# Performance work log

Hardware: AMD Instinct MI355X
Metric: run time of the kernel (lower is better)

Reference implementation:

```python
import jax, jax.numpy as jnp
import numpy as np
from jax import lax

EPS = 1e-5  # torch LayerNorm / BatchNorm1d default eps
HEADS, DH, DEPTH, C = 4, 128, 2, 512


def setup_inputs() -> dict:
    key = jax.random.key(0)
    ks = iter(jax.random.split(key, 48))
    def rn(shape, scale=1.0):
        return jax.random.normal(next(ks), shape, jnp.float32) * scale
    d, L = 1024, DEPTH
    inp = {}
    inp['x'] = rn((16, 10, 256, d))                      # (b, ncrops, T, d)
    # Temporal embedding: Conv1d(d -> 512, k=3, pad=1) + ReLU
    inp['W_emb'] = rn((C, d, 3), (d * 3) ** -0.5)
    inp['b_emb'] = jnp.zeros((C,), jnp.float32)
    # Transformer (depth=2), params stacked along layer axis
    inp['ln1_g'] = jnp.ones((L, C), jnp.float32); inp['ln1_b'] = jnp.zeros((L, C), jnp.float32)
    inp['W_qkv'] = rn((L, C, 4 * HEADS * DH), C ** -0.5)  # to_qkv (no bias), inner_dim*4 = 2048
    inp['W_o']  = rn((L, 2 * HEADS * DH, C), (2 * HEADS * DH) ** -0.5)
    inp['b_o']  = jnp.zeros((L, C), jnp.float32)
    inp['ln2_g'] = jnp.ones((L, C), jnp.float32); inp['ln2_b'] = jnp.zeros((L, C), jnp.float32)
    inp['W_f1'] = rn((L, C, C), C ** -0.5); inp['b_f1'] = jnp.zeros((L, C), jnp.float32)
    inp['W_f2'] = rn((L, C, C), C ** -0.5); inp['b_f2'] = jnp.zeros((L, C), jnp.float32)
    # NormalHead: conv1 512->32 (k=1), bn1, conv2 32->16 (k=1), bn2, conv3 16->1 (k=1)
    inp['c1_W'] = rn((32, C), C ** -0.5); inp['c1_b'] = jnp.zeros((32,), jnp.float32)
    inp['bn1_g'] = jnp.ones((32,), jnp.float32); inp['bn1_b'] = jnp.zeros((32,), jnp.float32)
    inp['bn1_m'] = rn((32,), 0.1)
    inp['bn1_v'] = jax.random.uniform(next(ks), (32,), jnp.float32, 0.5, 1.5)
    inp['c2_W'] = rn((16, 32), 32 ** -0.5); inp['c2_b'] = jnp.zeros((16,), jnp.float32)
    inp['bn2_g'] = jnp.ones((16,), jnp.float32); inp['bn2_b'] = jnp.zeros((16,), jnp.float32)
    inp['bn2_m'] = rn((16,), 0.1)
    inp['bn2_v'] = jax.random.uniform(next(ks), (16,), jnp.float32, 0.5, 1.5)
    inp['c3_W'] = rn((1, 16), 0.25); inp['c3_b'] = jnp.zeros((1,), jnp.float32)
    return inp


def _ln(z, g, b):
    m = z.mean(-1, keepdims=True)
    v = ((z - m) ** 2).mean(-1, keepdims=True)
    return (z - m) / jnp.sqrt(v + EPS) * g + b


def _bn_eval(z, g, b, m, v):  # z: (B, C, T), eval-mode BatchNorm1d
    return (z - m[None, :, None]) / jnp.sqrt(v[None, :, None] + EPS) * g[None, :, None] + b[None, :, None]


def _k1conv(z, W, b):  # pointwise Conv1d: z (B, Ci, T), W (Co, Ci)
    return jnp.einsum('bct,oc->bot', z, W) + b[None, :, None]


def reference(x, W_emb, b_emb, ln1_g, ln1_b, W_qkv, W_o, b_o, ln2_g, ln2_b,
              W_f1, b_f1, W_f2, b_f2, c1_W, c1_b, bn1_g, bn1_b, bn1_m, bn1_v,
              c2_W, c2_b, bn2_g, bn2_b, bn2_m, bn2_v, c3_W, c3_b):
    b, n, T, d = x.shape
    h = x.reshape(b * n, T, d)
    # Temporal embedding: Conv1d(k=3, pad=1) + ReLU
    h = lax.conv_general_dilated(h.transpose(0, 2, 1), W_emb, (1,), 'SAME',
                                 dimension_numbers=('NCH', 'OIH', 'NCH'))
    h = jax.nn.relu(h + b_emb[None, :, None]).transpose(0, 2, 1)  # (BN, T, 512)

    # fixed positional-decay attention map attn2 (T, T), batch-independent
    idx = jnp.arange(T, dtype=jnp.float32)
    tg = jnp.abs(idx[None, :] - idx[:, None])
    a2 = jnp.exp(-tg / jnp.exp(1.0))
    a2 = a2 / a2.sum(-1)  # NOTE: broadcast over last axis, exactly as in the torch code

    scale = DH ** -0.5
    for l in range(DEPTH):
        z = _ln(h, ln1_g[l], ln1_b[l])
        qkvt = z @ W_qkv[l]                                   # (BN, T, 2048)
        q, k, v, t = jnp.split(qkvt, 4, axis=-1)
        def to_heads(u):
            return u.reshape(u.shape[0], T, HEADS, DH).transpose(0, 2, 1, 3)
        q, k, v, t = map(to_heads, (q, k, v, t))              # (BN, H, T, DH)
        attn1 = jax.nn.softmax(jnp.einsum('bhid,bhjd->bhij', q, k) * scale, axis=-1)
        o1 = jnp.einsum('bhij,bhjd->bhid', attn1, v)
        o2 = jnp.einsum('ij,bhjd->bhid', a2, t)
        o = jnp.concatenate([o1, o2], axis=-1)                # (BN, H, T, 2*DH)
        o = o.transpose(0, 2, 1, 3).reshape(h.shape[0], T, HEADS * 2 * DH)
        h = o @ W_o[l] + b_o[l] + h                           # attn residual
        z = _ln(h, ln2_g[l], ln2_b[l])
        h = (jax.nn.gelu(z @ W_f1[l] + b_f1[l], approximate=False) @ W_f2[l] + b_f2[l]) + h

    # NormalHead on (BN, C, T)
    f = h.transpose(0, 2, 1)
    x1 = _k1conv(f, c1_W, c1_b)                               # (BN, 32, T)
    x2 = _k1conv(jax.nn.relu(_bn_eval(x1, bn1_g, bn1_b, bn1_m, bn1_v)), c2_W, c2_b)  # (BN, 16, T)
    scores = jax.nn.sigmoid(_k1conv(jax.nn.relu(_bn_eval(x2, bn2_g, bn2_b, bn2_m, bn2_v)), c3_W, c3_b))
    normal_scores = scores.reshape(b, n, T).mean(1)           # mean over ncrops -> (b, T)

    def maha(feats, anchor, var):  # Mahalanobis distance vs BN running stats (no eps, as in source)
        dist = jnp.sqrt(jnp.sum((feats - anchor[None, :, None]) ** 2 / var[None, :, None], axis=1))
        return dist.reshape(b, n, T).mean(1)

    distance_sum = maha(x1, bn1_m, bn1_v) + maha(x2, bn2_m, bn2_v)
    return distance_sum * normal_scores                       # (b, T)
```

## Files before the change

### kernel.cpp

```cpp
#include <hip/hip_runtime.h>
#include <math.h>

#define T_    256
#define D_    1024
#define C_    512
#define H_    4
#define DH_   128
#define BNB   160
#define LEPS  1e-5f
#define INV_E 0.36787944117144233f
#define SCALE_ 0.08838834764831845f
#define LDT   40

typedef unsigned short ushort;
typedef unsigned int   uint;
typedef __attribute__((ext_vector_type(8))) short short8;
typedef __attribute__((ext_vector_type(4))) float f32x4;

__device__ __forceinline__ ushort f2b(float f) {
    uint u = __float_as_uint(f);
    u += 0x7fffu + ((u >> 16) & 1u);
    return (ushort)(u >> 16);
}
__device__ __forceinline__ float b2f(ushort u) {
    return __uint_as_float(((uint)u) << 16);
}
__device__ __forceinline__ uint pk(float a, float b) {
    return (uint)f2b(a) | ((uint)f2b(b) << 16);
}

__global__ void zero_k(float* __restrict__ p, int n) {
    int i = blockIdx.x * 256 + threadIdx.x;
    if (i < n) p[i] = 0.0f;
}

__global__ void tconv_k(const float* __restrict__ src, ushort* __restrict__ dst,
                        int K, int N) {
    int idx = blockIdx.x * 256 + threadIdx.x;
    if (idx >= N * K) return;
    int n = idx / K, k = idx % K;
    dst[idx] = f2b(src[(size_t)k * N + n]);
}

__global__ void bcvt_k(const float* __restrict__ src, ushort* __restrict__ dst, int n) {
    int i = blockIdx.x * 256 + threadIdx.x;
    if (i < n) dst[i] = f2b(src[i]);
}

__global__ void wemb_k(const float* __restrict__ W, ushort* __restrict__ Wt) {
    int idx = blockIdx.x * 256 + threadIdx.x;
    if (idx >= C_ * 3072) return;
    int c = idx / 3072, k = idx % 3072;
    int dt = k >> 10, ci = k & 1023;
    Wt[idx] = f2b(W[(size_t)c * 3072 + ci * 3 + dt]);
}

__global__ void a2_colsum_k(float* __restrict__ s) {
    int j = threadIdx.x;
    float acc = 0.0f;
    for (int k = 0; k < T_; k++) acc += expf(-fabsf((float)(j - k)) * INV_E);
    s[j] = acc;
}

__global__ void a2fill_k(const float* __restrict__ s, ushort* __restrict__ A2) {
    int i = blockIdx.x, j = threadIdx.x;
    A2[i * 256 + j] = f2b(expf(-fabsf((float)(i - j)) * INV_E) / s[j]);
}

__global__ __launch_bounds__(256)
void ln_k(const float* __restrict__ X, const float* __restrict__ g,
          const float* __restrict__ b, ushort* __restrict__ Z) {
    int row = blockIdx.x;
    int tid = threadIdx.x;
    const float* xr = X + (size_t)row * C_;
    float x0 = xr[tid], x1 = xr[tid + 256];
    __shared__ float red[256];
    red[tid] = x0 + x1;
    __syncthreads();
    for (int s = 128; s >= 1; s >>= 1) {
        if (tid < s) red[tid] += red[tid + s];
        __syncthreads();
    }
    float mean = red[0] * (1.0f / C_);
    __syncthreads();
    float d0 = x0 - mean, d1 = x1 - mean;
    red[tid] = d0 * d0 + d1 * d1;
    __syncthreads();
    for (int s = 128; s >= 1; s >>= 1) {
        if (tid < s) red[tid] += red[tid + s];
        __syncthreads();
    }
    float rinv = rsqrtf(red[0] * (1.0f / C_) + LEPS);
    ushort* zr = Z + (size_t)row * C_;
    zr[tid]       = f2b(d0 * rinv * g[tid]       + b[tid]);
    zr[tid + 256] = f2b(d1 * rinv * g[tid + 256] + b[tid + 256]);
}

template<int CONV, int ACT, int RESID, int OUTBF>
__global__ __launch_bounds__(256)
void gemm_k(const ushort* __restrict__ A, const ushort* __restrict__ B,
            const float* __restrict__ bias, const float* __restrict__ R,
            void* __restrict__ Cout, int M, int N, int K,
            const float* __restrict__ Xf) {
    __shared__ __align__(16) ushort As[128 * LDT];
    __shared__ __align__(16) ushort Bs[128 * LDT];
    const int tid  = threadIdx.x;
    const int lane = tid & 63, wave = tid >> 6;
    const int wr = wave >> 1, wc = wave & 1;
    const int lm = lane & 15, quad = lane >> 4;
    const int m0 = blockIdx.y * 128, n0 = blockIdx.x * 128;
    const int r  = tid >> 1;
    const int c0 = (tid & 1) * 2;

    f32x4 acc[4][4];
#pragma unroll
    for (int mt = 0; mt < 4; mt++)
#pragma unroll
        for (int nt = 0; nt < 4; nt++) acc[mt][nt] = (f32x4){0.f, 0.f, 0.f, 0.f};

    for (int k0 = 0; k0 < K; k0 += 32) {
        if (CONV) {
            int g = m0 + r, bn = g >> 8, t = g & 255;
#pragma unroll
            for (int cc = 0; cc < 2; cc++) {
                int c = c0 + cc;
                int kc = k0 + c * 8;
                int dt = kc >> 10, ci = kc & 1023;
                int tt = t + dt - 1;
                uint4 val;
                if (tt >= 0 && tt < T_) {
                    const float* s = Xf + (size_t)(bn * T_ + tt) * D_ + ci;
                    float4 f0 = *(const float4*)s;
                    float4 f1 = *(const float4*)(s + 4);
                    val.x = pk(f0.x, f0.y); val.y = pk(f0.z, f0.w);
                    val.z = pk(f1.x, f1.y); val.w = pk(f1.z, f1.w);
                } else {
                    val.x = 0u; val.y = 0u; val.z = 0u; val.w = 0u;
                }
                *(uint4*)&As[r * LDT + c * 8] = val;
            }
        } else {
            const ushort* Arow = A + (size_t)(m0 + r) * K + k0;
            *(uint4*)&As[r * LDT + c0 * 8]       = *(const uint4*)(Arow + c0 * 8);
            *(uint4*)&As[r * LDT + (c0 + 1) * 8] = *(const uint4*)(Arow + (c0 + 1) * 8);
        }
        {
            const ushort* Brow = B + (size_t)(n0 + r) * K + k0;
            *(uint4*)&Bs[r * LDT + c0 * 8]       = *(const uint4*)(Brow + c0 * 8);
            *(uint4*)&Bs[r * LDT + (c0 + 1) * 8] = *(const uint4*)(Brow + (c0 + 1) * 8);
        }
        __syncthreads();
        short8 af[4], bfv[4];
#pragma unroll
        for (int mt = 0; mt < 4; mt++)
            af[mt] = *(const short8*)&As[(wr * 64 + mt * 16 + lm) * LDT + quad * 8];
#pragma unroll
        for (int nt = 0; nt < 4; nt++)
            bfv[nt] = *(const short8*)&Bs[(wc * 64 + nt * 16 + lm) * LDT + quad * 8];
#pragma unroll
        for (int mt = 0; mt < 4; mt++)
#pragma unroll
            for (int nt = 0; nt < 4; nt++)
                acc[mt][nt] = __builtin_amdgcn_mfma_f32_16x16x32_bf16(
                    af[mt], bfv[nt], acc[mt][nt], 0, 0, 0);
        __syncthreads();
    }

#pragma unroll
    for (int mt = 0; mt < 4; mt++) {
        int grow0 = m0 + wr * 64 + mt * 16 + quad * 4;
#pragma unroll
        for (int nt = 0; nt < 4; nt++) {
            int gcol = n0 + wc * 64 + nt * 16 + lm;
            float bia = bias ? bias[gcol] : 0.0f;
            f32x4 v = acc[mt][nt];
#pragma unroll
            for (int i = 0; i < 4; i++) {
                int grow = grow0 + i;
                float val = v[i] + bia;
                if (ACT == 1) val = val * 0.5f * (1.0f + erff(val * 0.70710678118654752f));
                if (ACT == 2) val = fmaxf(val, 0.0f);
                if (RESID) val += R[(size_t)grow * N + gcol];
                if (OUTBF) ((ushort*)Cout)[(size_t)grow * N + gcol] = f2b(val);
                else       ((float*)Cout)[(size_t)grow * N + gcol]  = val;
            }
        }
    }
}

__global__ __launch_bounds__(256)
void attn1_k(const ushort* __restrict__ qkvt, ushort* __restrict__ O) {
    const int bn = blockIdx.x, h = blockIdx.y;
    const int tid = threadIdx.x;
    const int wave = tid >> 6, lane = tid & 63;
    const int lm = lane & 15, quad = lane >> 4;
    __shared__ __align__(16) ushort Ks[32 * 136];
    __shared__ __align__(16) ushort Vt[128 * 40];
    __shared__ __align__(16) ushort Ps[4][64 * 40];
    const ushort* base = qkvt + (size_t)bn * T_ * 2048;

    short8 aq[4][4];
#pragma unroll
    for (int mt = 0; mt < 4; mt++) {
        const ushort* qrow = base + (size_t)(wave * 64 + mt * 16 + lm) * 2048 + h * DH_;
#pragma unroll
        for (int ks = 0; ks < 4; ks++)
            aq[mt][ks] = *(const short8*)(qrow + ks * 32 + quad * 8);
    }

    f32x4 oacc[4][8];
#pragma unroll
    for (int mt = 0; mt < 4; mt++)
#pragma unroll
        for (int nt = 0; nt < 8; nt++) oacc[mt][nt] = (f32x4){0.f, 0.f, 0.f, 0.f};
    float mrow[4][4], lrow[4][4];
#pragma unroll
    for (int mt = 0; mt < 4; mt++)
#pragma unroll
        for (int i = 0; i < 4; i++) { mrow[mt][i] = -1e30f; lrow[mt][i] = 0.0f; }

    for (int kt = 0; kt < 8; kt++) {
        __syncthreads();
#pragma unroll
        for (int u = 0; u < 2; u++) {
            int ii = tid + u * 256;
            int j = ii >> 4, dc = ii & 15;
            *(uint4*)&Ks[j * 136 + dc * 8] =
                *(const uint4*)(base + (size_t)(kt * 32 + j) * 2048 + 512 + h * DH_ + dc * 8);
        }
        {
            int j = tid & 31, half = tid >> 5;
            const ushort* vrow = base + (size_t)(kt * 32 + j) * 2048 + 1024 + h * DH_ + half * 16;
            uint4 v0 = *(const uint4*)vrow;
            uint4 v1 = *(const uint4*)(vrow + 8);
            ushort e[16];
            *(uint4*)&e[0] = v0; *(uint4*)&e[8] = v1;
#pragma unroll
            for (int u = 0; u < 16; u++)
                Vt[(half * 16 + u) * 40 + j] = e[u];
        }
        __syncthreads();

        f32x4 s[4][2];
#pragma unroll
        for (int mt = 0; mt < 4; mt++)
#pragma unroll
            for (int nt = 0; nt < 2; nt++) s[mt][nt] = (f32x4){0.f, 0.f, 0.f, 0.f};
#pragma unroll
        for (int ks = 0; ks < 4; ks++) {
            short8 bk0 = *(const short8*)&Ks[lm * 136 + ks * 32 + quad * 8];
            short8 bk1 = *(const short8*)&Ks[(16 + lm) * 136 + ks * 32 + quad * 8];
#pragma unroll
            for (int mt = 0; mt < 4; mt++) {
                s[mt][0] = __builtin_amdgcn_mfma_f32_16x16x32_bf16(aq[mt][ks], bk0, s[mt][0], 0, 0, 0);
                s[mt][1] = __builtin_amdgcn_mfma_f32_16x16x32_bf16(aq[mt][ks], bk1, s[mt][1], 0, 0, 0);
            }
        }

#pragma unroll
        for (int mt = 0; mt < 4; mt++) {
#pragma unroll
            for (int i = 0; i < 4; i++) {
                float v0 = s[mt][0][i] * SCALE_;
                float v1 = s[mt][1][i] * SCALE_;
                float rmax = fmaxf(v0, v1);
#pragma unroll
                for (int mk = 1; mk < 16; mk <<= 1)
                    rmax = fmaxf(rmax, __shfl_xor(rmax, mk));
                float mold = mrow[mt][i];
                float mnew = fmaxf(mold, rmax);
                float alpha = __expf(mold - mnew);
                float p0 = __expf(v0 - mnew);
                float p1 = __expf(v1 - mnew);
                float rs = p0 + p1;
#pragma unroll
                for (int mk = 1; mk < 16; mk <<= 1)
                    rs += __shfl_xor(rs, mk);
                lrow[mt][i] = lrow[mt][i] * alpha + rs;
                mrow[mt][i] = mnew;
#pragma unroll
                for (int nt = 0; nt < 8; nt++) {
                    oacc[mt][nt][i] *= alpha;
                }
                int prow = mt * 16 + quad * 4 + i;
                Ps[wave][prow * 40 + lm]      = f2b(p0);
                Ps[wave][prow * 40 + 16 + lm] = f2b(p1);
            }
        }

        short8 ap[4];
#pragma unroll
        for (int mt = 0; mt < 4; mt++)
            ap[mt] = *(const short8*)&Ps[wave][(mt * 16 + lm) * 40 + quad * 8];
#pragma unroll
        for (int nt = 0; nt < 8; nt++) {
            short8 bv = *(const short8*)&Vt[(nt * 16 + lm) * 40 + quad * 8];
#pragma unroll
            for (int mt = 0; mt < 4; mt++)
                oacc[mt][nt] = __builtin_amdgcn_mfma_f32_16x16x32_bf16(ap[mt], bv, oacc[mt][nt], 0, 0, 0);
        }
    }

#pragma unroll
    for (int mt = 0; mt < 4; mt++) {
#pragma unroll
        for (int i = 0; i < 4; i++) {
            int row = wave * 64 + mt * 16 + quad * 4 + i;
            float rinv = 1.0f / lrow[mt][i];
#pragma unroll
            for (int nt = 0; nt < 8; nt++) {
                int d = nt * 16 + lm;
                O[((size_t)bn * T_ + row) * 1024 + h * 256 + d] =
                    f2b(oacc[mt][nt][i] * rinv);
            }
        }
    }
}

__global__ __launch_bounds__(256)
void attn2_k(const ushort* __restrict__ A2, const ushort* __restrict__ qkvt,
             ushort* __restrict__ O) {
    __shared__ __align__(16) ushort As[128 * LDT];
    __shared__ __align__(16) ushort Bs[128 * 48];
    const int tid = threadIdx.x;
    const int bn = blockIdx.z;
    const int m0 = blockIdx.y * 128;
    const int n0 = blockIdx.x * 128;
    const int lane = tid & 63, wave = tid >> 6;
    const int wr = wave >> 1, wc = wave & 1;
    const int lm = lane & 15, quad = lane >> 4;
    const ushort* tbase = qkvt + (size_t)bn * T_ * 2048 + 1536;
    const int r = tid >> 1, c0 = (tid & 1) * 2;

    f32x4 acc[4][4];
#pragma unroll
    for (int mt = 0; mt < 4; mt++)
#pragma unroll
        for (int nt = 0; nt < 4; nt++) acc[mt][nt] = (f32x4){0.f, 0.f, 0.f, 0.f};

    for (int k0 = 0; k0 < 256; k0 += 32) {
        const ushort* Arow = A2 + (size_t)(m0 + r) * 256 + k0;
        *(uint4*)&As[r * LDT + c0 * 8]       = *(const uint4*)(Arow + c0 * 8);
        *(uint4*)&As[r * LDT + (c0 + 1) * 8] = *(const uint4*)(Arow + (c0 + 1) * 8);
        {
            int kr = tid & 31, np = tid >> 5;
            const ushort* trow = tbase + (size_t)(k0 + kr) * 2048 + n0 + np * 16;
            uint4 v0 = *(const uint4*)trow;
            uint4 v1 = *(const uint4*)(trow + 8);
            ushort e[16];
            *(uint4*)&e[0] = v0; *(uint4*)&e[8] = v1;
#pragma unroll
            for (int u = 0; u < 16; u++)
                Bs[(np * 16 + u) * 48 + kr] = e[u];
        }
        __syncthreads();
        short8 af[4], bf[4];
#pragma unroll
        for (int mt = 0; mt < 4; mt++)
            af[mt] = *(const short8*)&As[(wr * 64 + mt * 16 + lm) * LDT + quad * 8];
#pragma unroll
        for (int nt = 0; nt < 4; nt++)
            bf[nt] = *(const short8*)&Bs[(wc * 64 + nt * 16 + lm) * 48 + quad * 8];
#pragma unroll
        for (int mt = 0; mt < 4; mt++)
#pragma unroll
            for (int nt = 0; nt < 4; nt++)
                acc[mt][nt] = __builtin_amdgcn_mfma_f32_16x16x32_bf16(
                    af[mt], bf[nt], acc[mt][nt], 0, 0, 0);
        __syncthreads();
    }

#pragma unroll
    for (int mt = 0; mt < 4; mt++) {
        int row0 = m0 + wr * 64 + mt * 16 + quad * 4;
#pragma unroll
        for (int nt = 0; nt < 4; nt++) {
            int n = n0 + wc * 64 + nt * 16 + lm;
            int h = n >> 7, d = n & 127;
#pragma unroll
            for (int i = 0; i < 4; i++) {
                int row = row0 + i;
                O[((size_t)bn * T_ + row) * 1024 + h * 256 + 128 + d] =
                    f2b(acc[mt][nt][i]);
            }
        }
    }
}

#define BLD 520
__global__ __launch_bounds__(256)
void head1_k(const float* __restrict__ Hf, const ushort* __restrict__ c1Wb,
             const float* __restrict__ c1b, float* __restrict__ X1) {
    __shared__ __align__(16) ushort As[128 * LDT];
    __shared__ __align__(16) ushort Bs[32 * BLD];
    const int tid = threadIdx.x;
    const int lane = tid & 63, wave = tid >> 6;
    const int lm = lane & 15, quad = lane >> 4;
    const int m0 = blockIdx.x * 128;
#pragma unroll
    for (int u = 0; u < 8; u++) {
        int ii = tid + u * 256;
        int nrow = ii >> 6;
        int koff = (ii & 63) * 8;
        *(uint4*)&Bs[nrow * BLD + koff] = *(const uint4*)(c1Wb + nrow * 512 + koff);
    }
    f32x4 acc[2][2];
#pragma unroll
    for (int mt = 0; mt < 2; mt++)
#pragma unroll
        for (int nt = 0; nt < 2; nt++) acc[mt][nt] = (f32x4){0.f, 0.f, 0.f, 0.f};

    const int r = tid >> 1, half = tid & 1;
    for (int k0 = 0; k0 < 512; k0 += 32) {
        const float* s = Hf + (size_t)(m0 + r) * 512 + k0 + half * 16;
        float4 f0 = *(const float4*)s;
        float4 f1 = *(const float4*)(s + 4);
        float4 f2 = *(const float4*)(s + 8);
        float4 f3 = *(const float4*)(s + 12);
        uint4 v0, v1;
        v0.x = pk(f0.x, f0.y); v0.y = pk(f0.z, f0.w);
        v0.z = pk(f1.x, f1.y); v0.w = pk(f1.z, f1.w);
        v1.x = pk(f2.x, f2.y); v1.y = pk(f2.z, f2.w);
        v1.z = pk(f3.x, f3.y); v1.w = pk(f3.z, f3.w);
        __syncthreads();
        *(uint4*)&As[r * LDT + half * 16]     = v0;
        *(uint4*)&As[r * LDT + half * 16 + 8] = v1;
        __syncthreads();
        short8 af[2], bf[2];
#pragma unroll
        for (int mt = 0; mt < 2; mt++)
            af[mt] = *(const short8*)&As[(wave * 32 + mt * 16 + lm) * LDT + quad * 8];
#pragma unroll
        for (int nt = 0; nt < 2; nt++)
            bf[nt] = *(const short8*)&Bs[(nt * 16 + lm) * BLD + k0 + quad * 8];
#pragma unroll
        for (int mt = 0; mt < 2; mt++)
#pragma unroll
            for (int nt = 0; nt < 2; nt++)
                acc[mt][nt] = __builtin_amdgcn_mfma_f32_16x16x32_bf16(
                    af[mt], bf[nt], acc[mt][nt], 0, 0, 0);
    }
#pragma unroll
    for (int mt = 0; mt < 2; mt++) {
        int row0 = m0 + wave * 32 + mt * 16 + quad * 4;
#pragma unroll
        for (int nt = 0; nt < 2; nt++) {
            int col = nt * 16 + lm;
            float bia = c1b[col];
#pragma unroll
            for (int i = 0; i < 4; i++)
                X1[(size_t)(row0 + i) * 32 + col] = acc[mt][nt][i] + bia;
        }
    }
}

__global__ __launch_bounds__(256)
void head2_k(const float* __restrict__ X1, int bn_base, int M,
             const float* __restrict__ g1, const float* __restrict__ b1,
             const float* __restrict__ m1, const float* __restrict__ v1,
             const float* __restrict__ c2W, const float* __restrict__ c2b,
             const float* __restrict__ g2, const float* __restrict__ b2,
             const float* __restrict__ m2, const float* __restrict__ v2,
             const float* __restrict__ c3W, const float* __restrict__ c3b,
             float* __restrict__ sum_dist, float* __restrict__ sum_score) {
    int row = blockIdx.x * 256 + threadIdx.x;
    if (row >= M) return;
    float x1[32], y1[32];
    const float* xr = X1 + (size_t)row * 32;
#pragma unroll
    for (int c = 0; c < 32; c++) x1[c] = xr[c];
    float d1 = 0.0f;
#pragma unroll
    for (int c = 0; c < 32; c++) {
        float dd = x1[c] - m1[c];
        d1 += dd * dd / v1[c];
        y1[c] = fmaxf(0.0f, dd * rsqrtf(v1[c] + LEPS) * g1[c] + b1[c]);
    }
    float d2 = 0.0f, sc = c3b[0];
#pragma unroll
    for (int o = 0; o < 16; o++) {
        float acc = c2b[o];
        const float* wr = c2W + o * 32;
#pragma unroll
        for (int c = 0; c < 32; c++) acc += wr[c] * y1[c];
        float dd = acc - m2[o];
        d2 += dd * dd / v2[o];
        float y2 = fmaxf(0.0f, dd * rsqrtf(v2[o] + LEPS) * g2[o] + b2[o]);
        sc += c3W[o] * y2;
    }
    float dist = sqrtf(d1) + sqrtf(d2);
    sc = 1.0f / (1.0f + expf(-sc));
    int bn = bn_base + (row >> 8);
    int t = row & 255;
    int b = bn / 10;
    atomicAdd(&sum_dist[b * T_ + t], dist);
    atomicAdd(&sum_score[b * T_ + t], sc);
}

__global__ void combine_k(const float* __restrict__ sd, const float* __restrict__ ss,
                          float* __restrict__ out) {
    int i = blockIdx.x * 256 + threadIdx.x;
    if (i < 16 * T_) out[i] = (sd[i] * 0.1f) * (ss[i] * 0.1f);
}

extern "C" void kernel_launch(void* const* d_in, const int* in_sizes, int n_in,
                              void* d_out, int out_size, void* d_ws, size_t ws_size,
                              hipStream_t stream) {
    const float* x     = (const float*)d_in[0];
    const float* W_emb = (const float*)d_in[1];
    const float* b_emb = (const float*)d_in[2];
    const float* ln1_g = (const float*)d_in[3];
    const float* ln1_b = (const float*)d_in[4];
    const float* W_qkv = (const float*)d_in[5];
    const float* W_o   = (const float*)d_in[6];
    const float* b_o   = (const float*)d_in[7];
    const float* ln2_g = (const float*)d_in[8];
    const float* ln2_b = (const float*)d_in[9];
    const float* W_f1  = (const float*)d_in[10];
    const float* b_f1  = (const float*)d_in[11];
    const float* W_f2  = (const float*)d_in[12];
    const float* b_f2  = (const float*)d_in[13];
    const float* c1_W  = (const float*)d_in[14];
    const float* c1_b  = (const float*)d_in[15];
    const float* bn1_g = (const float*)d_in[16];
    const float* bn1_b = (const float*)d_in[17];
    const float* bn1_m = (const float*)d_in[18];
    const float* bn1_v = (const float*)d_in[19];
    const float* c2_W  = (const float*)d_in[20];
    const float* c2_b  = (const float*)d_in[21];
    const float* bn2_g = (const float*)d_in[22];
    const float* bn2_b = (const float*)d_in[23];
    const float* bn2_m = (const float*)d_in[24];
    const float* bn2_v = (const float*)d_in[25];
    const float* c3_W  = (const float*)d_in[26];
    const float* c3_b  = (const float*)d_in[27];
    float* out = (float*)d_out;

    char* p = (char*)d_ws;
    auto alloc = [&](size_t bytes) -> char* {
        char* q = p; p += (bytes + 255) & ~(size_t)255; return q;
    };
    ushort* wEmb = (ushort*)alloc((size_t)C_ * 3072 * 2);
    ushort* wQkv = (ushort*)alloc((size_t)2 * 2048 * 512 * 2);
    ushort* wO   = (ushort*)alloc((size_t)2 * 512 * 1024 * 2);
    ushort* wF1  = (ushort*)alloc((size_t)2 * 512 * 512 * 2);
    ushort* wF2  = (ushort*)alloc((size_t)2 * 512 * 512 * 2);
    ushort* A2bf = (ushort*)alloc((size_t)256 * 256 * 2);
    ushort* c1Wb = (ushort*)alloc((size_t)32 * 512 * 2);
    float*  s256      = (float*)alloc(256 * 4);
    float*  sum_dist  = (float*)alloc(4096 * 4);
    float*  sum_score = (float*)alloc(4096 * 4);
    size_t fixedB = (size_t)(p - (char*)d_ws);

    int CH = 8;
    const int cands[7] = {160, 80, 40, 32, 20, 16, 10};
    for (int ci = 0; ci < 7; ci++) {
        size_t per = (size_t)cands[ci] * 256 * 9344 + 4096;
        if (fixedB + per <= ws_size) { CH = cands[ci]; break; }
    }
    const int MR = CH * 256;
    float*  h    = (float*)alloc((size_t)MR * 512 * 4);
    ushort* z    = (ushort*)alloc((size_t)MR * 512 * 2);
    ushort* qkvt = (ushort*)alloc((size_t)MR * 2048 * 2);
    ushort* o    = (ushort*)alloc((size_t)MR * 1024 * 2);
    ushort* g    = o;
    float*  X1   = (float*)alloc((size_t)MR * 32 * 4);

    zero_k<<<(8192 + 255) / 256, 256, 0, stream>>>(sum_dist, 8192);
    a2_colsum_k<<<1, 256, 0, stream>>>(s256);
    a2fill_k<<<256, 256, 0, stream>>>(s256, A2bf);
    wemb_k<<<(C_ * 3072 + 255) / 256, 256, 0, stream>>>(W_emb, wEmb);
    bcvt_k<<<(32 * 512 + 255) / 256, 256, 0, stream>>>(c1_W, c1Wb, 32 * 512);
    for (int l = 0; l < 2; l++) {
        tconv_k<<<(2048 * 512 + 255) / 256, 256, 0, stream>>>(
            W_qkv + (size_t)l * 512 * 2048, wQkv + (size_t)l * 2048 * 512, 512, 2048);
        tconv_k<<<(512 * 1024 + 255) / 256, 256, 0, stream>>>(
            W_o + (size_t)l * 1024 * 512, wO + (size_t)l * 512 * 1024, 1024, 512);
        tconv_k<<<(512 * 512 + 255) / 256, 256, 0, stream>>>(
            W_f1 + (size_t)l * 512 * 512, wF1 + (size_t)l * 512 * 512, 512, 512);
        tconv_k<<<(512 * 512 + 255) / 256, 256, 0, stream>>>(
            W_f2 + (size_t)l * 512 * 512, wF2 + (size_t)l * 512 * 512, 512, 512);
    }

    for (int cs = 0; cs < BNB; cs += CH) {
        const float* xc = x + (size_t)cs * T_ * D_;

        gemm_k<1, 2, 0, 0><<<dim3(512 / 128, MR / 128), 256, 0, stream>>>(
            nullptr, wEmb, b_emb, nullptr, h, MR, 512, 3072, xc);

        for (int l = 0; l < 2; l++) {
            ln_k<<<MR, 256, 0, stream>>>(h, ln1_g + l * C_, ln1_b + l * C_, z);
            gemm_k<0, 0, 0, 1><<<dim3(2048 / 128, MR / 128), 256, 0, stream>>>(
                z, wQkv + (size_t)l * 2048 * 512, nullptr, nullptr, qkvt,
                MR, 2048, 512, nullptr);
            attn1_k<<<dim3(CH, H_), 256, 0, stream>>>(qkvt, o);
            attn2_k<<<dim3(4, 2, CH), 256, 0, stream>>>(A2bf, qkvt, o);
            gemm_k<0, 0, 1, 0><<<dim3(512 / 128, MR / 128), 256, 0, stream>>>(
                o, wO + (size_t)l * 512 * 1024, b_o + l * C_, h, h,
                MR, 512, 1024, nullptr);
            ln_k<<<MR, 256, 0, stream>>>(h, ln2_g + l * C_, ln2_b + l * C_, z);
            gemm_k<0, 1, 0, 1><<<dim3(512 / 128, MR / 128), 256, 0, stream>>>(
                z, wF1 + (size_t)l * 512 * 512, b_f1 + l * C_, nullptr, g,
                MR, 512, 512, nullptr);
            gemm_k<0, 0, 1, 0><<<dim3(512 / 128, MR / 128), 256, 0, stream>>>(
                g, wF2 + (size_t)l * 512 * 512, b_f2 + l * C_, h, h,
                MR, 512, 512, nullptr);
        }

        head1_k<<<MR / 128, 256, 0, stream>>>(h, c1Wb, c1_b, X1);
        head2_k<<<MR / 256, 256, 0, stream>>>(
            X1, cs, MR, bn1_g, bn1_b, bn1_m, bn1_v,
            c2_W, c2_b, bn2_g, bn2_b, bn2_m, bn2_v, c3_W, c3_b,
            sum_dist, sum_score);
    }

    combine_k<<<16, 256, 0, stream>>>(sum_dist, sum_score, out);
}
```

Measured before the change: 1.947 ms.

## Store residual stream in bf16 and pre-convert input x to bf16

The hidden-state residual buffer h becomes bf16 instead of fp32, so LayerNorm, the residual GEMM epilogues and head1 read and write half the bytes. The input x is converted to bf16 once per chunk by a new vectorized kernel, so the conv-embedding GEMM no longer re-reads and re-converts fp32 x for each of its three taps and every N tile. The trade-off is an extra full pass over x and a larger workspace, plus lower precision in the residual accumulation, which could affect accuracy.

```diff
diff --git a/kernel.cpp b/kernel.cpp
--- a/kernel.cpp
+++ b/kernel.cpp
@@ -34,6 +34,17 @@
     if (i < n) p[i] = 0.0f;
 }
 
+__global__ void xcvt_k(const float* __restrict__ src, ushort* __restrict__ dst, int n4) {
+    int i = blockIdx.x * 256 + threadIdx.x;
+    if (i < n4) {
+        float4 f = ((const float4*)src)[i];
+        uint2 v;
+        v.x = pk(f.x, f.y);
+        v.y = pk(f.z, f.w);
+        ((uint2*)dst)[i] = v;
+    }
+}
+
 __global__ void tconv_k(const float* __restrict__ src, ushort* __restrict__ dst,
                         int K, int N) {
     int idx = blockIdx.x * 256 + threadIdx.x;
@@ -68,12 +79,12 @@
 }
 
 __global__ __launch_bounds__(256)
-void ln_k(const float* __restrict__ X, const float* __restrict__ g,
+void ln_k(const ushort* __restrict__ X, const float* __restrict__ g,
           const float* __restrict__ b, ushort* __restrict__ Z) {
     int row = blockIdx.x;
     int tid = threadIdx.x;
-    const float* xr = X + (size_t)row * C_;
-    float x0 = xr[tid], x1 = xr[tid + 256];
+    const ushort* xr = X + (size_t)row * C_;
+    float x0 = b2f(xr[tid]), x1 = b2f(xr[tid + 256]);
     __shared__ float red[256];
     red[tid] = x0 + x1;
     __syncthreads();
@@ -99,9 +110,9 @@
 template<int CONV, int ACT, int RESID, int OUTBF>
 __global__ __launch_bounds__(256)
 void gemm_k(const ushort* __restrict__ A, const ushort* __restrict__ B,
-            const float* __restrict__ bias, const float* __restrict__ R,
+            const float* __restrict__ bias, const ushort* __restrict__ R,
             void* __restrict__ Cout, int M, int N, int K,
-            const float* __restrict__ Xf) {
+            const ushort* __restrict__ Xb) {
     __shared__ __align__(16) ushort As[128 * LDT];
     __shared__ __align__(16) ushort Bs[128 * LDT];
     const int tid  = threadIdx.x;
@@ -129,11 +140,7 @@
                 int tt = t + dt - 1;
                 uint4 val;
                 if (tt >= 0 && tt < T_) {
-                    const float* s = Xf + (size_t)(bn * T_ + tt) * D_ + ci;
-                    float4 f0 = *(const float4*)s;
-                    float4 f1 = *(const float4*)(s + 4);
-                    val.x = pk(f0.x, f0.y); val.y = pk(f0.z, f0.w);
-                    val.z = pk(f1.x, f1.y); val.w = pk(f1.z, f1.w);
+                    val = *(const uint4*)(Xb + ((size_t)bn * T_ + tt) * D_ + ci);
                 } else {
                     val.x = 0u; val.y = 0u; val.z = 0u; val.w = 0u;
                 }
@@ -180,7 +187,7 @@
                 float val = v[i] + bia;
                 if (ACT == 1) val = val * 0.5f * (1.0f + erff(val * 0.70710678118654752f));
                 if (ACT == 2) val = fmaxf(val, 0.0f);
-                if (RESID) val += R[(size_t)grow * N + gcol];
+                if (RESID) val += b2f(R[(size_t)grow * N + gcol]);
                 if (OUTBF) ((ushort*)Cout)[(size_t)grow * N + gcol] = f2b(val);
                 else       ((float*)Cout)[(size_t)grow * N + gcol]  = val;
             }
@@ -389,7 +396,7 @@
 
 #define BLD 520
 __global__ __launch_bounds__(256)
-void head1_k(const float* __restrict__ Hf, const ushort* __restrict__ c1Wb,
+void head1_k(const ushort* __restrict__ Hb, const ushort* __restrict__ c1Wb,
              const float* __restrict__ c1b, float* __restrict__ X1) {
     __shared__ __align__(16) ushort As[128 * LDT];
     __shared__ __align__(16) ushort Bs[32 * BLD];
@@ -412,16 +419,9 @@
 
     const int r = tid >> 1, half = tid & 1;
     for (int k0 = 0; k0 < 512; k0 += 32) {
-        const float* s = Hf + (size_t)(m0 + r) * 512 + k0 + half * 16;
-        float4 f0 = *(const float4*)s;
-        float4 f1 = *(const float4*)(s + 4);
-        float4 f2 = *(const float4*)(s + 8);
-        float4 f3 = *(const float4*)(s + 12);
-        uint4 v0, v1;
-        v0.x = pk(f0.x, f0.y); v0.y = pk(f0.z, f0.w);
-        v0.z = pk(f1.x, f1.y); v0.w = pk(f1.z, f1.w);
-        v1.x = pk(f2.x, f2.y); v1.y = pk(f2.z, f2.w);
-        v1.z = pk(f3.x, f3.y); v1.w = pk(f3.z, f3.w);
+        const ushort* s = Hb + (size_t)(m0 + r) * 512 + k0 + half * 16;
+        uint4 v0 = *(const uint4*)s;
+        uint4 v1 = *(const uint4*)(s + 8);
         __syncthreads();
         *(uint4*)&As[r * LDT + half * 16]     = v0;
         *(uint4*)&As[r * LDT + half * 16 + 8] = v1;
@@ -555,11 +555,12 @@
     int CH = 8;
     const int cands[7] = {160, 80, 40, 32, 20, 16, 10};
     for (int ci = 0; ci < 7; ci++) {
-        size_t per = (size_t)cands[ci] * 256 * 9344 + 4096;
+        size_t per = (size_t)cands[ci] * 256 * 10368 + 8192;
         if (fixedB + per <= ws_size) { CH = cands[ci]; break; }
     }
     const int MR = CH * 256;
-    float*  h    = (float*)alloc((size_t)MR * 512 * 4);
+    ushort* xb   = (ushort*)alloc((size_t)MR * 1024 * 2);
+    ushort* h    = (ushort*)alloc((size_t)MR * 512 * 2);
     ushort* z    = (ushort*)alloc((size_t)MR * 512 * 2);
     ushort* qkvt = (ushort*)alloc((size_t)MR * 2048 * 2);
     ushort* o    = (ushort*)alloc((size_t)MR * 1024 * 2);
@@ -585,8 +586,11 @@
     for (int cs = 0; cs < BNB; cs += CH) {
         const float* xc = x + (size_t)cs * T_ * D_;
 
-        gemm_k<1, 2, 0, 0><<<dim3(512 / 128, MR / 128), 256, 0, stream>>>(
-            nullptr, wEmb, b_emb, nullptr, h, MR, 512, 3072, xc);
+        int n4 = MR * 1024 / 4;
+        xcvt_k<<<(n4 + 255) / 256, 256, 0, stream>>>(xc, xb, n4);
+
+        gemm_k<1, 2, 0, 1><<<dim3(512 / 128, MR / 128), 256, 0, stream>>>(
+            nullptr, wEmb, b_emb, nullptr, h, MR, 512, 3072, xb);
 
         for (int l = 0; l < 2; l++) {
             ln_k<<<MR, 256, 0, stream>>>(h, ln1_g + l * C_, ln1_b + l * C_, z);
@@ -595,14 +599,14 @@
                 MR, 2048, 512, nullptr);
             attn1_k<<<dim3(CH, H_), 256, 0, stream>>>(qkvt, o);
             attn2_k<<<dim3(4, 2, CH), 256, 0, stream>>>(A2bf, qkvt, o);
-            gemm_k<0, 0, 1, 0><<<dim3(512 / 128, MR / 128), 256, 0, stream>>>(
+            gemm_k<0, 0, 1, 1><<<dim3(512 / 128, MR / 128), 256, 0, stream>>>(
                 o, wO + (size_t)l * 512 * 1024, b_o + l * C_, h, h,
                 MR, 512, 1024, nullptr);
             ln_k<<<MR, 256, 0, stream>>>(h, ln2_g + l * C_, ln2_b + l * C_, z);
             gemm_k<0, 1, 0, 1><<<dim3(512 / 128, MR / 128), 256, 0, stream>>>(
                 z, wF1 + (size_t)l * 512 * 512, b_f1 + l * C_, nullptr, g,
                 MR, 512, 512, nullptr);
-            gemm_k<0, 0, 1, 0><<<dim3(512 / 128, MR / 128), 256, 0, stream>>>(
+            gemm_k<0, 0, 1, 1><<<dim3(512 / 128, MR / 128), 256, 0, stream>>>(
                 g, wF2 + (size_t)l * 512 * 512, b_f2 + l * C_, h, h,
                 MR, 512, 512, nullptr);
         }
```

After: 1.841 ms. 5.5% less time.
